# Performance work log

Measured on AMD Instinct MI355X. Metric: run time of the kernel, lower is better.

The kernel has to match this reference:

```python
import jax, jax.numpy as jnp
import numpy as np

N_BINS = 229
OUT_F = 88
MODEL = 128
W_SIZE = 30
WIN = 2 * W_SIZE + 1  # 61


def _window(spec):
    B, T, F = spec.shape
    padded = jnp.pad(spec, ((0, 0), (W_SIZE, W_SIZE), (0, 0)))
    idx = jnp.arange(T)[:, None] + jnp.arange(WIN)[None, :]
    return padded[:, idx, :]


def setup_inputs() -> dict:
    key = jax.random.key(0)
    ks = jax.random.split(key, 12)
    B, T = 4, 1024
    s = 0.05
    return {
        "spec": jax.random.normal(ks[0], (B, T, N_BINS), dtype=jnp.float32),
        # frame_stack: Linear(N_BINS -> OUT_F)
        "W_frame": jax.random.normal(ks[1], (N_BINS, OUT_F), dtype=jnp.float32) * s,
        "b_frame": jnp.zeros((OUT_F,), dtype=jnp.float32),
        # onset attention: Linear(N_BINS + N_BINS -> MODEL), v: Linear(MODEL -> 1, no bias)
        "W_attn_o": jax.random.normal(ks[2], (2 * N_BINS, MODEL), dtype=jnp.float32) * s,
        "b_attn_o": jnp.zeros((MODEL,), dtype=jnp.float32),
        "v_o": jax.random.normal(ks[3], (MODEL,), dtype=jnp.float32) * s,
        # onset linear1: Linear(N_BINS -> OUT_F)
        "W_lin1": jax.random.normal(ks[4], (N_BINS, OUT_F), dtype=jnp.float32) * s,
        "b_lin1": jnp.zeros((OUT_F,), dtype=jnp.float32),
        # combine attention: Linear(2*OUT_F + N_BINS -> MODEL)
        "W_attn_c": jax.random.normal(ks[5], (2 * OUT_F + N_BINS, MODEL), dtype=jnp.float32) * s,
        "b_attn_c": jnp.zeros((MODEL,), dtype=jnp.float32),
        "v_c": jax.random.normal(ks[6], (MODEL,), dtype=jnp.float32) * s,
        # combine linear: Linear(2*OUT_F + N_BINS -> OUT_F)
        "W_linc": jax.random.normal(ks[7], (2 * OUT_F + N_BINS, OUT_F), dtype=jnp.float32) * s,
        "b_linc": jnp.zeros((OUT_F,), dtype=jnp.float32),
    }


def _attend(hidden, win, Wa, ba, v):
    B, T, Wn, F = win.shape
    h = jnp.broadcast_to(hidden[:, :, None, :], (B, T, Wn, hidden.shape[-1]))
    energy = jnp.tanh(jnp.concatenate([h, win], axis=-1) @ Wa + ba)
    scores = energy @ v
    return jax.nn.softmax(scores, axis=-1)


def reference(spec, W_frame, b_frame, W_attn_o, b_attn_o, v_o, W_lin1, b_lin1,
              W_attn_c, b_attn_c, v_c, W_linc, b_linc):
    win = _window(spec)

    feat_pred = spec @ W_frame + b_frame  # [B,T,OUT_F]

    # Onset stack
    a_onset = _attend(spec, win, W_attn_o, b_attn_o, v_o)
    weighted_o = jnp.einsum('btw,btwf->btf', a_onset, win)  # [B,T,N_BINS]
    onset_pred = jax.nn.sigmoid(weighted_o @ W_lin1 + b_lin1)  # [B,T,OUT_F]

    # Combine stack
    x = jnp.concatenate([feat_pred, onset_pred], axis=-1)  # [B,T,2*OUT_F]
    a_frame = _attend(x, win, W_attn_c, b_attn_c, v_c)
    weighted_c = jnp.einsum('btw,btwf->btf', a_frame, win)  # [B,T,N_BINS]
    frame_pred = jax.nn.sigmoid(jnp.concatenate([x, weighted_c], axis=-1) @ W_linc + b_linc)

    return (frame_pred, a_frame[:, :, None, :], onset_pred, a_onset[:, :, None, :], feat_pred)
```

## Files before the change

### kernel.cpp

```cpp
#include <hip/hip_runtime.h>

#define NBINS 229
#define OUTF  88
#define MODEL 128
#define WSZ   30
#define WIN   61
#define TLEN  1024
#define BT    4096

#define NC1 648
#define NP1 704
#define NC2 216

typedef short bf16x8 __attribute__((ext_vector_type(8)));
typedef float f32x4 __attribute__((ext_vector_type(4)));
typedef unsigned short ushort_t;

__device__ __forceinline__ float sigmoid_f(float x) {
    return __builtin_amdgcn_rcpf(1.f + __expf(-x));
}
__device__ __forceinline__ ushort_t f2bf(float f) {
    unsigned u = __float_as_uint(f);
    return (ushort_t)((u + 0x7fffu + ((u >> 16) & 1u)) >> 16);
}

__device__ __forceinline__ float dot8(uint4 pv, float4 ha, float4 hb,
                                      float4 va, float4 vb) {
    float r;
    r  = va.x * __builtin_amdgcn_rcpf(__builtin_fmaf(ha.x, __uint_as_float(pv.x << 16), 1.f));
    r += va.y * __builtin_amdgcn_rcpf(__builtin_fmaf(ha.y, __uint_as_float(pv.x & 0xffff0000u), 1.f));
    r += va.z * __builtin_amdgcn_rcpf(__builtin_fmaf(ha.z, __uint_as_float(pv.y << 16), 1.f));
    r += va.w * __builtin_amdgcn_rcpf(__builtin_fmaf(ha.w, __uint_as_float(pv.y & 0xffff0000u), 1.f));
    r += vb.x * __builtin_amdgcn_rcpf(__builtin_fmaf(hb.x, __uint_as_float(pv.z << 16), 1.f));
    r += vb.y * __builtin_amdgcn_rcpf(__builtin_fmaf(hb.y, __uint_as_float(pv.z & 0xffff0000u), 1.f));
    r += vb.z * __builtin_amdgcn_rcpf(__builtin_fmaf(hb.z, __uint_as_float(pv.w << 16), 1.f));
    r += vb.w * __builtin_amdgcn_rcpf(__builtin_fmaf(hb.w, __uint_as_float(pv.w & 0xffff0000u), 1.f));
    return r;
}

#define PREP_BLOCKS 1925

__global__ __launch_bounds__(256) void prep_kernel(
    const float* __restrict__ Wf,  const float* __restrict__ bfr,
    const float* __restrict__ Wao, const float* __restrict__ bao,
    const float* __restrict__ Wl1,
    const float* __restrict__ Wac, const float* __restrict__ bac,
    const float* __restrict__ Wlc,
    const float* __restrict__ spec,
    const float* __restrict__ vo, const float* __restrict__ vc,
    ushort_t* __restrict__ B1b, ushort_t* __restrict__ B2b,
    ushort_t* __restrict__ specB,
    float* __restrict__ bias1, float* __restrict__ bias2,
    float* __restrict__ sv)
{
    __shared__ float red[4];
    const int b = blockIdx.x;
    if (b < 704) {
        int idx = b * 256 + threadIdx.x;
        int n = idx >> 8, k = idx & 255;
        float v = 0.f;
        if (k < NBINS && n < NC1) {
            if (n < 88)       v = Wf[k * 88 + n];
            else if (n < 216) v = Wao[k * MODEL + (n - 88)];
            else if (n < 344) v = Wao[(k + NBINS) * MODEL + (n - 216)];
            else if (n < 472) v = Wac[(k + 176) * MODEL + (n - 344)];
            else if (n < 560) v = Wl1[k * 88 + (n - 472)];
            else              v = Wlc[(k + 176) * 88 + (n - 560)];
        }
        B1b[idx] = f2bf(v);
    } else if (b < 896) {
        int idx = (b - 704) * 256 + threadIdx.x;
        int n = idx / 192, k = idx - n * 192;
        float v = 0.f;
        if (k < 176 && n < NC2)
            v = (n < 128) ? Wac[k * MODEL + n] : Wlc[k * 88 + (n - 128)];
        B2b[idx] = f2bf(v);
    } else if (b < 1920) {
        int idx = (b - 896) * 256 + threadIdx.x;
        int r = idx >> 6, k4 = (idx & 63) * 4;
        const float* sp = spec + (size_t)r * NBINS;
        ushort4 o;
        o.x = (k4 + 0 < NBINS) ? f2bf(sp[k4 + 0]) : (ushort_t)0;
        o.y = (k4 + 1 < NBINS) ? f2bf(sp[k4 + 1]) : (ushort_t)0;
        o.z = (k4 + 2 < NBINS) ? f2bf(sp[k4 + 2]) : (ushort_t)0;
        o.w = (k4 + 3 < NBINS) ? f2bf(sp[k4 + 3]) : (ushort_t)0;
        *(ushort4*)&specB[(size_t)r * 256 + k4] = o;
    } else if (b < 1924) {
        int idx = (b - 1920) * 256 + threadIdx.x;
        if (idx < 704)
            bias1[idx] = (idx < 88) ? bfr[idx] : (idx < 216 ? bao[idx - 88] : 0.f);
        else if (idx < 960) {
            int n = idx - 704;
            bias2[n] = (n < 128) ? bac[n] : 0.f;
        }
    } else {
        int wid = threadIdx.x >> 6, lane = threadIdx.x & 63;
        const float* vp = (wid < 2) ? vo : vc;
        float val = vp[(wid & 1) * 64 + lane];
#pragma unroll
        for (int m = 32; m; m >>= 1) val += __shfl_xor(val, m, 64);
        if (lane == 0) red[wid] = val;
        __syncthreads();
        if (threadIdx.x == 0) {
            sv[0] = red[0] + red[1];
            sv[1] = red[2] + red[3];
        }
    }
}

template<int KITER, int RTS>
__global__ __launch_bounds__(256) void gemm_mfma(
    const ushort_t* __restrict__ Ab, int lka,
    const ushort_t* __restrict__ Bb,
    const float* __restrict__ bias, int Nc,
    float* __restrict__ feat, float* __restrict__ EHo_,
    ushort_t* __restrict__ EPo_, ushort_t* __restrict__ EPc_,
    ushort_t* __restrict__ Rb_, ushort_t* __restrict__ Qb_)
{
    const int tid = threadIdx.x;
    const int wv = tid >> 6, ln = tid & 63;
    const int l15 = ln & 15, qd = ln >> 4;
    const int flat = blockIdx.y * gridDim.x + blockIdx.x;
    const int e = flat & 7, kf = flat >> 3;
    const int rb = (e * (1 << RTS) + (kf & ((1 << RTS) - 1))) * 64;
    const int cb = (kf >> RTS) * 64;
    const int lkb = KITER * 32;

    const ushort_t* ap = Ab + (size_t)(rb + wv * 16 + l15) * lka + qd * 8;
    const ushort_t* bp[4];
#pragma unroll
    for (int nt = 0; nt < 4; nt++)
        bp[nt] = Bb + (size_t)(cb + nt * 16 + l15) * lkb + qd * 8;

    f32x4 acc[4];
#pragma unroll
    for (int nt = 0; nt < 4; nt++) acc[nt] = (f32x4){0.f, 0.f, 0.f, 0.f};

    bf16x8 af = *(const bf16x8*)ap, bfv[4];
#pragma unroll
    for (int nt = 0; nt < 4; nt++) bfv[nt] = *(const bf16x8*)bp[nt];

    for (int it = 0; it < KITER; it++) {
        bf16x8 an, bn[4];
        const int nk = (it + 1 < KITER) ? (it + 1) * 32 : 0;
        an = *(const bf16x8*)(ap + nk);
#pragma unroll
        for (int nt = 0; nt < 4; nt++) bn[nt] = *(const bf16x8*)(bp[nt] + nk);
#pragma unroll
        for (int nt = 0; nt < 4; nt++)
            acc[nt] = __builtin_amdgcn_mfma_f32_16x16x32_bf16(
                af, bfv[nt], acc[nt], 0, 0, 0);
        af = an;
#pragma unroll
        for (int nt = 0; nt < 4; nt++) bfv[nt] = bn[nt];
    }

    const int mbase = rb + wv * 16 + qd * 4;
#pragma unroll
    for (int nt = 0; nt < 4; nt++) {
        const int n = cb + nt * 16 + l15;
        if (n < Nc) {
            const float bn = bias[n];
#pragma unroll
            for (int r = 0; r < 4; r++) {
                const int m = mbase + r;
                float val = acc[nt][r] + bn;
                if (n < 88) {
                    feat[(size_t)m * 88 + n] = val;
                } else if (n < 216) {
                    EHo_[(size_t)m * 128 + (n - 88)] = __expf(val + val);
                } else if (n < 344) {
                    EPo_[(size_t)m * 128 + (n - 216)] = f2bf(__expf(val + val));
                } else if (n < 472) {
                    EPc_[(size_t)m * 128 + (n - 344)] = f2bf(__expf(val + val));
                } else if (n < 560) {
                    Rb_[(size_t)m * 96 + (n - 472)] = f2bf(val);
                } else {
                    Qb_[(size_t)m * 96 + (n - 560)] = f2bf(val);
                }
            }
        }
    }
}

#define EPST 136
#define RST  96
#define XST  200

__global__ __launch_bounds__(512) void attn_fused(
    const float* __restrict__ EHo,
    const ushort_t* __restrict__ EPo_g,
    const ushort_t* __restrict__ Rb,
    const ushort_t* __restrict__ EPc_g,
    const ushort_t* __restrict__ Qb,
    const float* __restrict__ feat,
    const ushort_t* __restrict__ B2b,
    const float* __restrict__ bias2,
    const float* __restrict__ vo, const float* __restrict__ vc,
    const float* __restrict__ svp,
    const float* __restrict__ bl1, const float* __restrict__ blc,
    float* __restrict__ a_o_out, float* __restrict__ onset_out,
    float* __restrict__ a_c_out, float* __restrict__ frame_out)
{
    __shared__ alignas(16) ushort_t Plo[68 * EPST];
    __shared__ alignas(16) ushort_t Rl [68 * RST];
    __shared__ alignas(16) ushort_t Plc[68 * EPST];
    __shared__ alignas(16) ushort_t Ql [68 * RST];
    __shared__ alignas(16) ushort_t Xb [16 * XST];
    __shared__ alignas(16) float    EHc[8 * 128];
    __shared__ alignas(16) float    basec[8 * 88];

    const int tid = threadIdx.x;
    const int s0 = ((blockIdx.x & 7) * 64 + (blockIdx.x >> 3)) * 8;
    const int t0 = s0 & (TLEN - 1);

    for (int i = tid; i < 68 * 16; i += 512) {
        int j = i >> 4, c = (i & 15) * 8;
        int tg = t0 + j - WSZ;
        uint4 vP = {0x3f803f80u, 0x3f803f80u, 0x3f803f80u, 0x3f803f80u};
        uint4 vC = vP;
        if ((unsigned)tg < (unsigned)TLEN) {
            vP = *(const uint4*)&EPo_g[(size_t)(s0 - WSZ + j) * 128 + c];
            vC = *(const uint4*)&EPc_g[(size_t)(s0 - WSZ + j) * 128 + c];
        }
        *(uint4*)&Plo[j * EPST + c] = vP;
        *(uint4*)&Plc[j * EPST + c] = vC;
    }
    for (int i = tid; i < 68 * 12; i += 512) {
        int j = i / 12, c = (i - j * 12) * 8;
        int tg = t0 + j - WSZ;
        uint4 vR = {0u, 0u, 0u, 0u}, vQ = {0u, 0u, 0u, 0u};
        if ((unsigned)tg < (unsigned)TLEN) {
            vR = *(const uint4*)&Rb[(size_t)(s0 - WSZ + j) * 96 + c];
            vQ = *(const uint4*)&Qb[(size_t)(s0 - WSZ + j) * 96 + c];
        }
        *(uint4*)&Rl[j * RST + c] = vR;
        *(uint4*)&Ql[j * RST + c] = vQ;
    }
    for (int i = tid; i < 16 * XST; i += 512) {
        int r = i / XST, k = i - r * XST;
        ushort_t v = 0;
        if (r < 8 && k < 88) v = f2bf(feat[(size_t)(s0 + r) * 88 + k]);
        Xb[i] = v;
    }
    __syncthreads();

    const int q = tid >> 6;
    const int w = tid & 63;
    const int s = s0 + q;
    const int su = __builtin_amdgcn_readfirstlane(s);
    const int row = q + ((w < WIN) ? w : 0);

    {
        const ushort_t* pb = &Plo[row * EPST];
        const float* hrow = EHo + (size_t)su * 128;
        float accr = 0.f;
#pragma unroll
        for (int d8 = 0; d8 < 16; d8++) {
            uint4 pv = *(const uint4*)(pb + d8 * 8);
            float4 ha = *(const float4*)(hrow + d8 * 8);
            float4 hb = *(const float4*)(hrow + d8 * 8 + 4);
            float4 va = *(const float4*)(vo + d8 * 8);
            float4 vb = *(const float4*)(vo + d8 * 8 + 4);
            accr += dot8(pv, ha, hb, va, vb);
        }
        float eng = svp[0] - 2.f * accr;
        if (w >= WIN) eng = -1e30f;

        float mx = eng;
#pragma unroll
        for (int m = 32; m; m >>= 1) mx = fmaxf(mx, __shfl_xor(mx, m, 64));
        float ex = __expf(eng - mx);
        float sm = ex;
#pragma unroll
        for (int m = 32; m; m >>= 1) sm += __shfl_xor(sm, m, 64);
        float a = ex * __builtin_amdgcn_rcpf(sm);
        if (w < WIN) a_o_out[(size_t)s * WIN + w] = a;

        if (w < 44) {
            const int f = 2 * w;
            float acc0 = bl1[f], acc1 = bl1[f + 1];
            const ushort_t* rr0 = &Rl[q * RST + f];
#pragma unroll
            for (int ww = 0; ww < WIN; ww++) {
                float aw = __uint_as_float(
                    __builtin_amdgcn_readlane(__float_as_uint(a), ww));
                unsigned u = *(const unsigned*)(rr0 + ww * RST);
                acc0 += aw * __uint_as_float(u << 16);
                acc1 += aw * __uint_as_float(u & 0xffff0000u);
            }
            float p0 = sigmoid_f(acc0), p1 = sigmoid_f(acc1);
            *(float2*)&onset_out[(size_t)s * OUTF + f] = make_float2(p0, p1);
            ushort2 o; o.x = f2bf(p0); o.y = f2bf(p1);
            *(ushort2*)&Xb[q * XST + 88 + f] = o;
        }
    }
    __syncthreads();

    {
        const int l15 = w & 15, qd = w >> 4;
#pragma unroll
        for (int rt = 0; rt < 2; rt++) {
            const int t = q + rt * 8;
            if (t < 14) {
                const int n0 = t * 16;
                const ushort_t* bp = B2b + (size_t)(n0 + l15) * 192 + qd * 8;
                const ushort_t* ap = &Xb[l15 * XST + qd * 8];
                f32x4 acc = (f32x4){0.f, 0.f, 0.f, 0.f};
#pragma unroll
                for (int it = 0; it < 6; it++) {
                    bf16x8 av = *(const bf16x8*)(ap + it * 32);
                    bf16x8 bv = *(const bf16x8*)(bp + it * 32);
                    acc = __builtin_amdgcn_mfma_f32_16x16x32_bf16(
                        av, bv, acc, 0, 0, 0);
                }
                if (qd < 2) {
                    const int n = n0 + l15;
                    const float b2 = bias2[n];
#pragma unroll
                    for (int r = 0; r < 4; r++) {
                        const int m = qd * 4 + r;
                        float val = acc[r] + b2;
                        if (n < 128)        EHc[m * 128 + n] = __expf(val + val);
                        else if (n < NC2)   basec[m * 88 + (n - 128)] = val;
                    }
                }
            }
        }
    }
    __syncthreads();

    {
        const ushort_t* pb = &Plc[row * EPST];
        const float* hl = &EHc[q * 128];
        float accr = 0.f;
#pragma unroll
        for (int d8 = 0; d8 < 16; d8++) {
            uint4 pv = *(const uint4*)(pb + d8 * 8);
            float4 ha = *(const float4*)(hl + d8 * 8);
            float4 hb = *(const float4*)(hl + d8 * 8 + 4);
            float4 va = *(const float4*)(vc + d8 * 8);
            float4 vb = *(const float4*)(vc + d8 * 8 + 4);
            accr += dot8(pv, ha, hb, va, vb);
        }
        float eng = svp[1] - 2.f * accr;
        if (w >= WIN) eng = -1e30f;

        float mx = eng;
#pragma unroll
        for (int m = 32; m; m >>= 1) mx = fmaxf(mx, __shfl_xor(mx, m, 64));
        float ex = __expf(eng - mx);
        float sm = ex;
#pragma unroll
        for (int m = 32; m; m >>= 1) sm += __shfl_xor(sm, m, 64);
        float a = ex * __builtin_amdgcn_rcpf(sm);
        if (w < WIN) a_c_out[(size_t)s * WIN + w] = a;

        if (w < 44) {
            const int f = 2 * w;
            float acc0 = blc[f]     + basec[q * 88 + f];
            float acc1 = blc[f + 1] + basec[q * 88 + f + 1];
            const ushort_t* rr0 = &Ql[q * RST + f];
#pragma unroll
            for (int ww = 0; ww < WIN; ww++) {
                float aw = __uint_as_float(
                    __builtin_amdgcn_readlane(__float_as_uint(a), ww));
                unsigned u = *(const unsigned*)(rr0 + ww * RST);
                acc0 += aw * __uint_as_float(u << 16);
                acc1 += aw * __uint_as_float(u & 0xffff0000u);
            }
            float p0 = sigmoid_f(acc0), p1 = sigmoid_f(acc1);
            *(float2*)&frame_out[(size_t)s * OUTF + f] = make_float2(p0, p1);
        }
    }
}

extern "C" void kernel_launch(void* const* d_in, const int* in_sizes, int n_in,
                              void* d_out, int out_size, void* d_ws, size_t ws_size,
                              hipStream_t stream)
{
    const float* spec = (const float*)d_in[0];
    const float* Wf   = (const float*)d_in[1];
    const float* bf_  = (const float*)d_in[2];
    const float* Wao  = (const float*)d_in[3];
    const float* bao  = (const float*)d_in[4];
    const float* vo   = (const float*)d_in[5];
    const float* Wl1  = (const float*)d_in[6];
    const float* bl1  = (const float*)d_in[7];
    const float* Wac  = (const float*)d_in[8];
    const float* bac  = (const float*)d_in[9];
    const float* vc   = (const float*)d_in[10];
    const float* Wlc  = (const float*)d_in[11];
    const float* blc  = (const float*)d_in[12];

    float* out  = (float*)d_out;
    float* out0 = out;
    float* out1 = out + 360448;
    float* out2 = out + 610304;
    float* out3 = out + 970752;
    float* out4 = out + 1220608;

    float* ws = (float*)d_ws;
    float*    sv    = ws;
    float*    bias1 = ws + 16;
    float*    bias2 = ws + 720;
    ushort_t* B1b   = (ushort_t*)(ws + 976);
    ushort_t* B2b   = (ushort_t*)(ws + 91088);
    ushort_t* specB = (ushort_t*)(ws + 115664);
    float*    EHo   = ws + 639952;
    ushort_t* EPo   = (ushort_t*)(ws + 1164240);
    ushort_t* EPc   = (ushort_t*)(ws + 1426384);
    ushort_t* Rb    = (ushort_t*)(ws + 1688528);
    ushort_t* Qb    = (ushort_t*)(ws + 1885136);
    (void)ws_size; (void)in_sizes; (void)n_in; (void)out_size;

    prep_kernel<<<PREP_BLOCKS, 256, 0, stream>>>(
        Wf, bf_, Wao, bao, Wl1, Wac, bac, Wlc, spec, vo, vc,
        B1b, B2b, specB, bias1, bias2, sv);

    gemm_mfma<8, 3><<<dim3(NP1 / 64, 64), 256, 0, stream>>>(
        specB, 256, B1b, bias1, NC1, out4, EHo, EPo, EPc, Rb, Qb);

    attn_fused<<<BT / 8, 512, 0, stream>>>(
        EHo, EPo, Rb, EPc, Qb, out4, B2b, bias2, vo, vc, sv, bl1, blc,
        out3, out2, out1, out0);
}
```

Before: 126.3 us.

## Fuse spec bf16 conversion into GEMM A-loads and swizzle attention LDS rows

The GEMM now reads fp32 spec directly and converts it to bf16 in registers, with guarded tail handling at the 229-column boundary. This removes the prep pass that wrote a padded bf16 copy of spec, along with its workspace buffer. Separately, the EPo/EPc shared-memory tiles in the attention kernel get an XOR swizzle on 16-byte chunks keyed by row to reduce LDS bank conflicts. In exchange, the GEMM A-loads become unaligned fp32 reads (row stride 229) that are reconverted by each of the column-tile blocks.

```diff
diff --git a/kernel.cpp b/kernel.cpp
--- a/kernel.cpp
+++ b/kernel.cpp
@@ -38,7 +38,7 @@
     return r;
 }
 
-#define PREP_BLOCKS 1925
+#define PREP_BLOCKS 901
 
 __global__ __launch_bounds__(256) void prep_kernel(
     const float* __restrict__ Wf,  const float* __restrict__ bfr,
@@ -46,10 +46,8 @@
     const float* __restrict__ Wl1,
     const float* __restrict__ Wac, const float* __restrict__ bac,
     const float* __restrict__ Wlc,
-    const float* __restrict__ spec,
     const float* __restrict__ vo, const float* __restrict__ vc,
     ushort_t* __restrict__ B1b, ushort_t* __restrict__ B2b,
-    ushort_t* __restrict__ specB,
     float* __restrict__ bias1, float* __restrict__ bias2,
     float* __restrict__ sv)
 {
@@ -75,18 +73,8 @@
         if (k < 176 && n < NC2)
             v = (n < 128) ? Wac[k * MODEL + n] : Wlc[k * 88 + (n - 128)];
         B2b[idx] = f2bf(v);
-    } else if (b < 1920) {
+    } else if (b < 900) {
         int idx = (b - 896) * 256 + threadIdx.x;
-        int r = idx >> 6, k4 = (idx & 63) * 4;
-        const float* sp = spec + (size_t)r * NBINS;
-        ushort4 o;
-        o.x = (k4 + 0 < NBINS) ? f2bf(sp[k4 + 0]) : (ushort_t)0;
-        o.y = (k4 + 1 < NBINS) ? f2bf(sp[k4 + 1]) : (ushort_t)0;
-        o.z = (k4 + 2 < NBINS) ? f2bf(sp[k4 + 2]) : (ushort_t)0;
-        o.w = (k4 + 3 < NBINS) ? f2bf(sp[k4 + 3]) : (ushort_t)0;
-        *(ushort4*)&specB[(size_t)r * 256 + k4] = o;
-    } else if (b < 1924) {
-        int idx = (b - 1920) * 256 + threadIdx.x;
         if (idx < 704)
             bias1[idx] = (idx < 88) ? bfr[idx] : (idx < 216 ? bao[idx - 88] : 0.f);
         else if (idx < 960) {
@@ -108,9 +96,29 @@
     }
 }
 
+__device__ __forceinline__ bf16x8 cvt8(f32x4 a, f32x4 b) {
+    bf16x8 r;
+    r[0] = (short)f2bf(a.x); r[1] = (short)f2bf(a.y);
+    r[2] = (short)f2bf(a.z); r[3] = (short)f2bf(a.w);
+    r[4] = (short)f2bf(b.x); r[5] = (short)f2bf(b.y);
+    r[6] = (short)f2bf(b.z); r[7] = (short)f2bf(b.w);
+    return r;
+}
+__device__ __forceinline__ bf16x8 loadA(const float* sp, int k0) {
+    if (k0 > 228) return (bf16x8)(short)0;
+    f32x4 a, b;
+    __builtin_memcpy(&a, sp + k0, 16);
+    if (k0 <= 216) {
+        __builtin_memcpy(&b, sp + k0 + 4, 16);
+    } else {
+        b = (f32x4){sp[228], 0.f, 0.f, 0.f};
+    }
+    return cvt8(a, b);
+}
+
 template<int KITER, int RTS>
 __global__ __launch_bounds__(256) void gemm_mfma(
-    const ushort_t* __restrict__ Ab, int lka,
+    const float* __restrict__ spec,
     const ushort_t* __restrict__ Bb,
     const float* __restrict__ bias, int Nc,
     float* __restrict__ feat, float* __restrict__ EHo_,
@@ -126,7 +134,7 @@
     const int cb = (kf >> RTS) * 64;
     const int lkb = KITER * 32;
 
-    const ushort_t* ap = Ab + (size_t)(rb + wv * 16 + l15) * lka + qd * 8;
+    const float* sp = spec + (size_t)(rb + wv * 16 + l15) * NBINS;
     const ushort_t* bp[4];
 #pragma unroll
     for (int nt = 0; nt < 4; nt++)
@@ -136,14 +144,14 @@
 #pragma unroll
     for (int nt = 0; nt < 4; nt++) acc[nt] = (f32x4){0.f, 0.f, 0.f, 0.f};
 
-    bf16x8 af = *(const bf16x8*)ap, bfv[4];
+    bf16x8 af = loadA(sp, qd * 8), bfv[4];
 #pragma unroll
     for (int nt = 0; nt < 4; nt++) bfv[nt] = *(const bf16x8*)bp[nt];
 
     for (int it = 0; it < KITER; it++) {
         bf16x8 an, bn[4];
         const int nk = (it + 1 < KITER) ? (it + 1) * 32 : 0;
-        an = *(const bf16x8*)(ap + nk);
+        an = loadA(sp, nk + qd * 8);
 #pragma unroll
         for (int nt = 0; nt < 4; nt++) bn[nt] = *(const bf16x8*)(bp[nt] + nk);
 #pragma unroll
@@ -216,6 +224,7 @@
 
     for (int i = tid; i < 68 * 16; i += 512) {
         int j = i >> 4, c = (i & 15) * 8;
+        int cs = ((i & 15) ^ ((j >> 3) & 7)) * 8;
         int tg = t0 + j - WSZ;
         uint4 vP = {0x3f803f80u, 0x3f803f80u, 0x3f803f80u, 0x3f803f80u};
         uint4 vC = vP;
@@ -223,8 +232,8 @@
             vP = *(const uint4*)&EPo_g[(size_t)(s0 - WSZ + j) * 128 + c];
             vC = *(const uint4*)&EPc_g[(size_t)(s0 - WSZ + j) * 128 + c];
         }
-        *(uint4*)&Plo[j * EPST + c] = vP;
-        *(uint4*)&Plc[j * EPST + c] = vC;
+        *(uint4*)&Plo[j * EPST + cs] = vP;
+        *(uint4*)&Plc[j * EPST + cs] = vC;
     }
     for (int i = tid; i < 68 * 12; i += 512) {
         int j = i / 12, c = (i - j * 12) * 8;
@@ -250,6 +259,7 @@
     const int s = s0 + q;
     const int su = __builtin_amdgcn_readfirstlane(s);
     const int row = q + ((w < WIN) ? w : 0);
+    const int rsw = (row >> 3) & 7;
 
     {
         const ushort_t* pb = &Plo[row * EPST];
@@ -257,7 +267,7 @@
         float accr = 0.f;
 #pragma unroll
         for (int d8 = 0; d8 < 16; d8++) {
-            uint4 pv = *(const uint4*)(pb + d8 * 8);
+            uint4 pv = *(const uint4*)(pb + ((d8 ^ rsw) << 3));
             float4 ha = *(const float4*)(hrow + d8 * 8);
             float4 hb = *(const float4*)(hrow + d8 * 8 + 4);
             float4 va = *(const float4*)(vo + d8 * 8);
@@ -336,7 +346,7 @@
         float accr = 0.f;
 #pragma unroll
         for (int d8 = 0; d8 < 16; d8++) {
-            uint4 pv = *(const uint4*)(pb + d8 * 8);
+            uint4 pv = *(const uint4*)(pb + ((d8 ^ rsw) << 3));
             float4 ha = *(const float4*)(hl + d8 * 8);
             float4 hb = *(const float4*)(hl + d8 * 8 + 4);
             float4 va = *(const float4*)(vc + d8 * 8);
@@ -406,20 +416,19 @@
     float*    bias2 = ws + 720;
     ushort_t* B1b   = (ushort_t*)(ws + 976);
     ushort_t* B2b   = (ushort_t*)(ws + 91088);
-    ushort_t* specB = (ushort_t*)(ws + 115664);
-    float*    EHo   = ws + 639952;
-    ushort_t* EPo   = (ushort_t*)(ws + 1164240);
-    ushort_t* EPc   = (ushort_t*)(ws + 1426384);
-    ushort_t* Rb    = (ushort_t*)(ws + 1688528);
-    ushort_t* Qb    = (ushort_t*)(ws + 1885136);
+    float*    EHo   = ws + 115664;
+    ushort_t* EPo   = (ushort_t*)(ws + 639952);
+    ushort_t* EPc   = (ushort_t*)(ws + 902096);
+    ushort_t* Rb    = (ushort_t*)(ws + 1164240);
+    ushort_t* Qb    = (ushort_t*)(ws + 1360848);
     (void)ws_size; (void)in_sizes; (void)n_in; (void)out_size;
 
     prep_kernel<<<PREP_BLOCKS, 256, 0, stream>>>(
-        Wf, bf_, Wao, bao, Wl1, Wac, bac, Wlc, spec, vo, vc,
-        B1b, B2b, specB, bias1, bias2, sv);
+        Wf, bf_, Wao, bao, Wl1, Wac, bac, Wlc, vo, vc,
+        B1b, B2b, bias1, bias2, sv);
 
     gemm_mfma<8, 3><<<dim3(NP1 / 64, 64), 256, 0, stream>>>(
-        specB, 256, B1b, bias1, NC1, out4, EHo, EPo, EPc, Rb, Qb);
+        spec, B1b, bias1, NC1, out4, EHo, EPo, EPc, Rb, Qb);
 
     attn_fused<<<BT / 8, 512, 0, stream>>>(
         EHo, EPo, Rb, EPc, Qb, out4, B2b, bias2, vo, vc, sv, bl1, blc,
```

New measurement: 123.5 us. 2.2% less time.
